# Optimization experiments

Hardware: AMD Instinct MI355X
Metric: run time of the kernel (lower is better)

The kernel has to match this reference:

```python
import jax, jax.numpy as jnp
import numpy as np

N_HEADS = 16
D_HEAD = 64
CHUNK = 64


@jax.custom_vjp
def binarize(x):
    return jnp.where(x >= 0, 1.0, -1.0).astype(x.dtype)

def _bin_fwd(x):
    return binarize(x), x

def _bin_bwd(x, g):
    return (g * (jnp.abs(x) <= 1.0).astype(g.dtype),)

binarize.defvjp(_bin_fwd, _bin_bwd)


def setup_inputs() -> dict:
    key = jax.random.key(0)
    k1, k2, k3 = jax.random.split(key, 3)
    B, T, D = 4, 4096, 1024
    x = jax.random.normal(k1, (B, T, D), dtype=jnp.float32)
    W_qkv = jax.random.normal(k2, (3 * D, D), dtype=jnp.float32) * 0.02
    W_o = jax.random.normal(k3, (D, D), dtype=jnp.float32) * 0.02
    return {"x": x, "W_qkv": W_qkv, "W_o": W_o}


def reference(x, W_qkv, W_o):
    B, T, D = x.shape
    H, d, C = N_HEADS, D_HEAD, CHUNK
    scale = 1.0 / (d ** 0.5)

    qkv = (x @ W_qkv.T).reshape(B, T, 3, H, d)
    q = jnp.swapaxes(qkv[:, :, 0], 1, 2) * scale   # [B,H,T,d]
    k = binarize(jnp.swapaxes(qkv[:, :, 1], 1, 2))
    v = binarize(jnp.swapaxes(qkv[:, :, 2], 1, 2))

    N = T // C  # T chosen divisible by chunk size (pad branch is a no-op)
    qc = q.reshape(B, H, N, C, d)
    kc = k.reshape(B, H, N, C, d)
    vc = v.reshape(B, H, N, C, d)

    mask = jnp.tril(jnp.ones((C, C), dtype=x.dtype))
    intra_scores = jnp.einsum('bhnid,bhnjd->bhnij', qc, kc) * mask
    intra = jnp.einsum('bhnij,bhnjd->bhnid', intra_scores, vc)

    chunk_kv = jnp.einsum('bhnck,bhncd->bhnkd', kc, vc)          # [B,H,N,d,d]
    ckv32 = chunk_kv.astype(jnp.float32)
    prefix = (jnp.cumsum(ckv32, axis=2) - ckv32).astype(chunk_kv.dtype)
    cross = jnp.einsum('bhnck,bhnkd->bhncd', qc, prefix)

    pos = jnp.arange(1, C + 1, dtype=x.dtype)
    offs = jnp.arange(N, dtype=x.dtype) * C
    total = jnp.clip(offs[:, None] + pos[None, :], 1.0, None).reshape(1, 1, N, C, 1)

    out = ((intra + cross) / total).reshape(B, H, T, d)
    out = jnp.swapaxes(out, 1, 2).reshape(B, T, D)
    y = out @ W_o.T

    final_matrix = prefix[:, :, -1] + chunk_kv[:, :, -1]          # [B,H,d,d]
    final_count = jnp.full((B, H, 1, 1), T, dtype=x.dtype)
    return (y, final_matrix, final_count)
```

## Files before the change

### kernel.cpp

```cpp
#include <hip/hip_runtime.h>
#include <cstdint>

#define B_ 4
#define T_ 4096
#define D_ 1024
#define H_ 16
#define HD_ 64
#define N_ 64

typedef __attribute__((ext_vector_type(8))) short s16x8;
typedef __attribute__((ext_vector_type(4))) float f32x4;

__device__ __forceinline__ unsigned short f2bf(float f) {
    unsigned int u = __builtin_bit_cast(unsigned int, f);
    u += 0x7fffu + ((u >> 16) & 1u);
    return (unsigned short)(u >> 16);
}
__device__ __forceinline__ float bf2f(unsigned short h) {
    unsigned int u = ((unsigned int)h) << 16;
    return __builtin_bit_cast(float, u);
}
__device__ __forceinline__ void gl2lds(const short* g, short* l) {
    __builtin_amdgcn_global_load_lds(
        (const __attribute__((address_space(1))) void*)g,
        (__attribute__((address_space(3))) void*)l, 16, 0, 0);
}
#define MFMA16(a, b, c) __builtin_amdgcn_mfma_f32_16x16x32_bf16(a, b, c, 0, 0, 0)
#define SB0() __builtin_amdgcn_sched_barrier(0)
#define BAR() __builtin_amdgcn_s_barrier()

#define BF_P1 ((short)0x3F80)
#define BF_M1 ((short)0xBF80)

__global__ __launch_bounds__(256)
void k_cvt(const float* __restrict__ in, short* __restrict__ out, int n4)
{
    int i = blockIdx.x * blockDim.x + threadIdx.x;
    const int stride = gridDim.x * blockDim.x;
    for (; i < n4; i += stride) {
        float4 f = ((const float4*)in)[i];
        short4 o;
        o.x = (short)f2bf(f.x); o.y = (short)f2bf(f.y);
        o.z = (short)f2bf(f.z); o.w = (short)f2bf(f.w);
        *(short4*)(out + i * 4) = o;
    }
}

template<int MODE, int KD, int NCB>
__global__ __launch_bounds__(512, 4)
void k_gemm2(const short* __restrict__ A, const short* __restrict__ Bm,
             short* __restrict__ Oq, signed char* __restrict__ K8,
             signed char* __restrict__ V8, float* __restrict__ Yf)
{
    __shared__ __align__(16) short LA[256 * 64];
    __shared__ __align__(16) short LB[128 * 64];

    const int tid = threadIdx.x;
    const int nwg = 64 * NCB;
    const int bid = blockIdx.x;
    const int sz  = (bid & 7) * (nwg >> 3) + (bid >> 3);
    const int cb  = sz % NCB, rb = sz / NCB;
    const int row0 = rb * 256, col0 = cb * 128;

    const int lane = tid & 63, w = tid >> 6;
    const int wr = w >> 1, wc = w & 1;
    const int cl = lane & 15, rg = lane >> 4;

    const int sr8 = lane >> 3;
    const int slg = ((lane & 7) ^ sr8) * 8;
    const short* gA = A  + (size_t)(row0 + w * 32 + sr8) * KD + slg;
    const short* gB = Bm + (size_t)(col0 + w * 16 + sr8) * KD + slg;

    f32x4 acc[4][4];
    #pragma unroll
    for (int i = 0; i < 4; ++i)
        #pragma unroll
        for (int j = 0; j < 4; ++j) acc[i][j] = (f32x4)0.f;

    auto stage = [&](int t) {
        const int ko = t * 64;
        #pragma unroll
        for (int c = 0; c < 4; ++c)
            gl2lds(gA + ko + (size_t)c * 8 * KD, &LA[(w * 32 + c * 8) * 64]);
        #pragma unroll
        for (int c = 0; c < 2; ++c)
            gl2lds(gB + ko + (size_t)c * 8 * KD, &LB[(w * 16 + c * 8) * 64]);
    };
    auto ldf = [&](const short* base, int R, int q) -> s16x8 {
        return *(const s16x8*)((const char*)base + R * 128 + ((q ^ (R & 7)) << 4));
    };

    const int nt = KD / 64;
    stage(0);
    for (int t = 0; t < nt; ++t) {
        asm volatile("s_waitcnt vmcnt(0)" ::: "memory");
        BAR();
        SB0();
        #pragma unroll
        for (int kk = 0; kk < 2; ++kk) {
            s16x8 fb[4];
            #pragma unroll
            for (int ni = 0; ni < 4; ++ni)
                fb[ni] = ldf(LB, wc * 64 + ni * 16 + cl, kk * 4 + rg);
            #pragma unroll
            for (int mi = 0; mi < 4; ++mi) {
                s16x8 fa = ldf(LA, wr * 64 + mi * 16 + cl, kk * 4 + rg);
                __builtin_amdgcn_s_setprio(1);
                #pragma unroll
                for (int ni = 0; ni < 4; ++ni)
                    acc[mi][ni] = MFMA16(fa, fb[ni], acc[mi][ni]);
                __builtin_amdgcn_s_setprio(0);
            }
        }
        SB0();
        BAR();
        if (t + 1 < nt) stage(t + 1);
    }

    const int m0 = row0 + wr * 64, n0 = col0 + wc * 64;
    if (MODE == 0) {
        const int s = col0 >> 10;
        #pragma unroll
        for (int ni = 0; ni < 4; ++ni) {
            const int col = n0 + ni * 16 + cl;
            const int h = (col & 1023) >> 6, dd = col & 63;
            #pragma unroll
            for (int mi = 0; mi < 4; ++mi)
                #pragma unroll
                for (int r = 0; r < 4; ++r) {
                    const int bt = m0 + mi * 16 + rg * 4 + r;
                    const int bb = bt >> 12, t = bt & (T_ - 1);
                    const size_t bh64 = (size_t)(bb * H_ + h);
                    const float v = acc[mi][ni][r];
                    if (s == 0) {
                        Oq[(bh64 * T_ + t) * 64 + dd] =
                            (short)f2bf(v * 0.125f);
                    } else if (s == 1) {
                        K8[(bh64 * T_ + t) * 64 + dd] =
                            (v >= 0.f) ? 1 : -1;
                    } else {
                        const size_t otr = bh64 * ((size_t)T_ * 64)
                                         + (size_t)(t >> 6) * 4096 + dd * 64 + (t & 63);
                        V8[otr] = (v >= 0.f) ? 1 : -1;
                    }
                }
        }
    } else {
        #pragma unroll
        for (int ni = 0; ni < 4; ++ni) {
            const int col = n0 + ni * 16 + cl;
            #pragma unroll
            for (int mi = 0; mi < 4; ++mi)
                #pragma unroll
                for (int r = 0; r < 4; ++r)
                    Yf[(size_t)(m0 + mi * 16 + rg * 4 + r) * D_ + col] =
                        acc[mi][ni][r];
        }
    }
}

__global__ __launch_bounds__(256)
void k_chunkA(const signed char* __restrict__ Kb8,
              const signed char* __restrict__ VbT8,
              signed char* __restrict__ CKV8)
{
    __shared__ __align__(16) short KTs[4096], VTs[4096];
    __shared__ __align__(16) signed char Cs8[4096];
    const int tid = threadIdx.x;
    const int bh = blockIdx.x >> 6, n = blockIdx.x & 63;
    const size_t kbase = ((size_t)bh * T_ + n * 64) * 64;
    const size_t vbase = (size_t)bh * T_ * 64 + (size_t)n * 4096;

    {
        const int off = tid * 16;
        int4 vr = *(const int4*)(VbT8 + vbase + off);
        const signed char* vb = (const signed char*)&vr;
        const int vrow = off >> 6, vcb = off & 63;
        #pragma unroll
        for (int jj = 0; jj < 2; ++jj) {
            s16x8 v;
            #pragma unroll
            for (int j = 0; j < 8; ++j)
                v[j] = (vb[jj*8+j] >= 0) ? BF_P1 : BF_M1;
            const int o = (vrow * 128 + (vcb + jj * 8) * 2) ^ ((vrow & 7) << 4);
            *(s16x8*)((char*)VTs + o) = v;
        }
        int4 kr = *(const int4*)(Kb8 + kbase + off);
        const signed char* kb = (const signed char*)&kr;
        const int c = off >> 6, d0 = off & 63;
        #pragma unroll
        for (int j = 0; j < 16; ++j) {
            const int dd = d0 + j;
            const short sv = (kb[j] >= 0) ? BF_P1 : BF_M1;
            const int o2 = (dd * 128 + c * 2) ^ ((dd & 7) << 4);
            *(short*)((char*)KTs + o2) = sv;
        }
    }
    __syncthreads();

    const int lane = tid & 63, w = tid >> 6;
    const int cl = lane & 15, rg = lane >> 4;
    auto frag = [&](const short* l, int rowbase, int kk) -> s16x8 {
        const int row = rowbase + cl;
        int off = row * 128 + kk * 64 + rg * 16;
        off ^= (row & 7) << 4;
        return *(const s16x8*)((const char*)l + off);
    };

    f32x4 a3[4];
    #pragma unroll
    for (int ni = 0; ni < 4; ++ni) a3[ni] = (f32x4)0.f;
    const s16x8 va0 = frag(VTs, w * 16, 0), va1 = frag(VTs, w * 16, 1);
    #pragma unroll
    for (int ni = 0; ni < 4; ++ni) {
        a3[ni] = MFMA16(va0, frag(KTs, ni * 16, 0), a3[ni]);
        a3[ni] = MFMA16(va1, frag(KTs, ni * 16, 1), a3[ni]);
    }
    #pragma unroll
    for (int ni = 0; ni < 4; ++ni)
        #pragma unroll
        for (int r = 0; r < 4; ++r) {
            const int m = w * 16 + rg * 4 + r;
            const int c = ni * 16 + cl;
            Cs8[m * 64 + c] = (signed char)(int)a3[ni][r];
        }
    __syncthreads();
    const size_t c8 = ((size_t)bh * 64 + n) * 4096;
    *(int4*)(CKV8 + c8 + tid * 16) = *(const int4*)(Cs8 + tid * 16);
}

__global__ __launch_bounds__(256)
void k_scan2(const signed char* __restrict__ CKV8, short* __restrict__ PB,
             float* __restrict__ FM, float* __restrict__ FC)
{
    const int bh = blockIdx.x >> 4;
    const int e  = (blockIdx.x & 15) * 256 + threadIdx.x;
    const size_t b8 = (size_t)bh * N_ * 4096 + e;
    const size_t bp = (size_t)bh * N_ * 4096 + e;
    int run = 0;
    #pragma unroll
    for (int nn = 0; nn < 64; ++nn) {
        PB[bp + (size_t)nn * 4096] = (short)f2bf((float)run);
        run += (int)CKV8[b8 + (size_t)nn * 4096];
    }
    FM[(size_t)bh * 4096 + (e & 63) * 64 + (e >> 6)] = (float)run;
    if ((blockIdx.x & 15) == 0 && threadIdx.x == 0) FC[bh] = (float)T_;
}

__global__ __launch_bounds__(256)
void k_cross3(const short* __restrict__ Qb, const signed char* __restrict__ Kb8,
              const signed char* __restrict__ VbT8, const short* __restrict__ PB,
              short* __restrict__ OMb)
{
    __shared__ __align__(16) short Qs[4096], Ks[4096], VTs[4096], Ps[4096], Ss[4096];
    const int tid = threadIdx.x;
    const int bh = blockIdx.x >> 6, n = blockIdx.x & 63;
    const size_t cbase = ((size_t)bh * T_ + n * 64) * 64;
    const size_t kbase = cbase;
    const size_t vbase = (size_t)bh * T_ * 64 + (size_t)n * 4096;

    auto stage_tile = [&](const short* g, short* l) {
        #pragma unroll
        for (int p = 0; p < 2; ++p) {
            const int off = tid * 16 + p * 4096;
            const int r = off >> 7;
            s16x8 v = *(const s16x8*)(g + (off >> 1));
            *(s16x8*)((char*)l + (off ^ ((r & 7) << 4))) = v;
        }
    };
    stage_tile(Qb + cbase, Qs);
    stage_tile(PB + ((size_t)bh * 64 + n) * 4096, Ps);
    {
        const int off = tid * 16;
        int4 kr = *(const int4*)(Kb8 + kbase + off);
        const signed char* kb = (const signed char*)&kr;
        int4 vr = *(const int4*)(VbT8 + vbase + off);
        const signed char* vb = (const signed char*)&vr;
        const int row = off >> 6, cb = off & 63;
        #pragma unroll
        for (int jj = 0; jj < 2; ++jj) {
            s16x8 kv, vv;
            #pragma unroll
            for (int j = 0; j < 8; ++j) {
                kv[j] = (kb[jj*8+j] >= 0) ? BF_P1 : BF_M1;
                vv[j] = (vb[jj*8+j] >= 0) ? BF_P1 : BF_M1;
            }
            const int o = (row * 128 + (cb + jj * 8) * 2) ^ ((row & 7) << 4);
            *(s16x8*)((char*)Ks  + o) = kv;
            *(s16x8*)((char*)VTs + o) = vv;
        }
    }
    __syncthreads();

    const int lane = tid & 63, w = tid >> 6;
    const int cl = lane & 15, rg = lane >> 4;
    auto frag = [&](const short* l, int rowbase, int kk) -> s16x8 {
        const int row = rowbase + cl;
        int off = row * 128 + kk * 64 + rg * 16;
        off ^= (row & 7) << 4;
        return *(const s16x8*)((const char*)l + off);
    };

    const s16x8 qa0 = frag(Qs, w * 16, 0), qa1 = frag(Qs, w * 16, 1);
    {
        f32x4 a1[4];
        #pragma unroll
        for (int ni = 0; ni < 4; ++ni) a1[ni] = (f32x4)0.f;
        #pragma unroll
        for (int ni = 0; ni < 4; ++ni) {
            a1[ni] = MFMA16(qa0, frag(Ks, ni * 16, 0), a1[ni]);
            a1[ni] = MFMA16(qa1, frag(Ks, ni * 16, 1), a1[ni]);
        }
        #pragma unroll
        for (int ni = 0; ni < 4; ++ni)
            #pragma unroll
            for (int r = 0; r < 4; ++r) {
                const int i = w * 16 + rg * 4 + r, j = ni * 16 + cl;
                const float v = (j <= i) ? a1[ni][r] : 0.f;
                const int off = (i * 128 + j * 2) ^ ((i & 7) << 4);
                *(short*)((char*)Ss + off) = (short)f2bf(v);
            }
    }
    __syncthreads();

    {
        f32x4 a2[4], a3[4];
        #pragma unroll
        for (int ni = 0; ni < 4; ++ni) { a2[ni] = (f32x4)0.f; a3[ni] = (f32x4)0.f; }
        const s16x8 sa0 = frag(Ss, w * 16, 0), sa1 = frag(Ss, w * 16, 1);
        #pragma unroll
        for (int ni = 0; ni < 4; ++ni) {
            a2[ni] = MFMA16(sa0, frag(VTs, ni * 16, 0), a2[ni]);
            a2[ni] = MFMA16(sa1, frag(VTs, ni * 16, 1), a2[ni]);
            a3[ni] = MFMA16(qa0, frag(Ps, ni * 16, 0), a3[ni]);
            a3[ni] = MFMA16(qa1, frag(Ps, ni * 16, 1), a3[ni]);
        }
        #pragma unroll
        for (int ni = 0; ni < 4; ++ni)
            #pragma unroll
            for (int r = 0; r < 4; ++r) {
                const int i = w * 16 + rg * 4 + r, j = ni * 16 + cl;
                const float invt = 1.0f / (float)(n * 64 + i + 1);
                const float f = (a2[ni][r] + a3[ni][r]) * invt;
                const int off = (i * 128 + j * 2) ^ ((i & 7) << 4);
                *(short*)((char*)Qs + off) = (short)f2bf(f);
            }
    }
    __syncthreads();

    const int bb = bh >> 4, h = bh & 15;
    #pragma unroll
    for (int p = 0; p < 2; ++p) {
        const int off = tid * 16 + p * 4096;
        const int r = off >> 7;
        const int lo = off ^ ((r & 7) << 4);
        s16x8 v = *(const s16x8*)((char*)Qs + lo);
        const size_t gi = ((size_t)bb * T_ + n * 64 + r) * D_
                        + h * 64 + ((off & 127) >> 1);
        *(s16x8*)(OMb + gi) = v;
    }
}

extern "C" void kernel_launch(void* const* d_in, const int* in_sizes, int n_in,
                              void* d_out, int out_size, void* d_ws, size_t ws_size,
                              hipStream_t stream)
{
    const float* X    = (const float*)d_in[0];
    const float* Wqkv = (const float*)d_in[1];
    const float* Wo   = (const float*)d_in[2];

    float* Y  = (float*)d_out;
    float* FM = Y + (size_t)B_ * T_ * D_;
    float* FC = FM + (size_t)B_ * H_ * HD_ * HD_;

    char* ws = (char*)d_ws;
    const size_t Mi = 1048576;
    short*       Qb     = (short*)(ws + 0 * Mi);
    signed char* Kb8    = (signed char*)(ws + 32 * Mi);
    signed char* VbT8   = (signed char*)(ws + 48 * Mi);
    short*       PB     = (short*)(ws + 64 * Mi);
    short*       Xb     = (short*)(ws + 96 * Mi);
    short*       OMb    = (short*)(ws + 96 * Mi);
    signed char* CKV8   = (signed char*)(ws + 128 * Mi);
    short*       Wqkvb  = (short*)(ws + 144 * Mi);
    short*       WoS    = (short*)(ws + 150 * Mi);
    if (ws_size < (size_t)152 * Mi) return;

    dim3 blk(256), blkg(512);
    k_cvt<<<dim3(2048), blk, 0, stream>>>(X, Xb, 4194304);
    k_cvt<<<dim3(1024), blk, 0, stream>>>(Wqkv, Wqkvb, 786432);
    k_gemm2<0, 1024, 24><<<dim3(1536), blkg, 0, stream>>>(Xb, Wqkvb, Qb, Kb8, VbT8, nullptr);
    k_chunkA<<<dim3(4096), blk, 0, stream>>>(Kb8, VbT8, CKV8);
    k_scan2 <<<dim3(1024), blk, 0, stream>>>(CKV8, PB, FM, FC);
    k_cross3<<<dim3(4096), blk, 0, stream>>>(Qb, Kb8, VbT8, PB, OMb);
    k_cvt<<<dim3(512), blk, 0, stream>>>(Wo, WoS, 262144);
    k_gemm2<1, 1024, 8><<<dim3(512), blkg, 0, stream>>>(OMb, WoS, nullptr, nullptr, nullptr, Y);
}
```

Before: 261.6 us.

## Double-buffer GEMM LDS tiles and shrink to 128x128 tiles with 256 threads

The GEMM kernel moves from a 256x128 tile with 512 threads and a single LDS buffer to a 128x128 tile with 256 threads and two LDS buffers. The next K-slice is loaded into the alternate buffer before waiting, with a partial vmcnt wait, so global-to-LDS loads overlap MFMA work. Grid sizes double to cover the smaller tiles. This trades larger-tile reuse and lower occupancy (launch bounds 256,2) for load/compute overlap.

```diff
diff --git a/kernel.cpp b/kernel.cpp
--- a/kernel.cpp
+++ b/kernel.cpp
@@ -47,20 +47,19 @@
 }
 
 template<int MODE, int KD, int NCB>
-__global__ __launch_bounds__(512, 4)
-void k_gemm2(const short* __restrict__ A, const short* __restrict__ Bm,
+__global__ __launch_bounds__(256, 2)
+void k_gemm3(const short* __restrict__ A, const short* __restrict__ Bm,
              short* __restrict__ Oq, signed char* __restrict__ K8,
              signed char* __restrict__ V8, float* __restrict__ Yf)
 {
-    __shared__ __align__(16) short LA[256 * 64];
-    __shared__ __align__(16) short LB[128 * 64];
+    __shared__ __align__(16) short LS[2][2][8192];
 
     const int tid = threadIdx.x;
-    const int nwg = 64 * NCB;
+    const int nwg = 128 * NCB;
     const int bid = blockIdx.x;
     const int sz  = (bid & 7) * (nwg >> 3) + (bid >> 3);
     const int cb  = sz % NCB, rb = sz / NCB;
-    const int row0 = rb * 256, col0 = cb * 128;
+    const int row0 = rb * 128, col0 = cb * 128;
 
     const int lane = tid & 63, w = tid >> 6;
     const int wr = w >> 1, wc = w & 1;
@@ -69,7 +68,7 @@
     const int sr8 = lane >> 3;
     const int slg = ((lane & 7) ^ sr8) * 8;
     const short* gA = A  + (size_t)(row0 + w * 32 + sr8) * KD + slg;
-    const short* gB = Bm + (size_t)(col0 + w * 16 + sr8) * KD + slg;
+    const short* gB = Bm + (size_t)(col0 + w * 32 + sr8) * KD + slg;
 
     f32x4 acc[4][4];
     #pragma unroll
@@ -77,34 +76,41 @@
         #pragma unroll
         for (int j = 0; j < 4; ++j) acc[i][j] = (f32x4)0.f;
 
-    auto stage = [&](int t) {
+    auto stage = [&](int pb, int t) {
         const int ko = t * 64;
         #pragma unroll
-        for (int c = 0; c < 4; ++c)
-            gl2lds(gA + ko + (size_t)c * 8 * KD, &LA[(w * 32 + c * 8) * 64]);
-        #pragma unroll
-        for (int c = 0; c < 2; ++c)
-            gl2lds(gB + ko + (size_t)c * 8 * KD, &LB[(w * 16 + c * 8) * 64]);
+        for (int c = 0; c < 4; ++c) {
+            gl2lds(gA + ko + (size_t)c * 8 * KD, &LS[pb][0][(w * 32 + c * 8) * 64]);
+            gl2lds(gB + ko + (size_t)c * 8 * KD, &LS[pb][1][(w * 32 + c * 8) * 64]);
+        }
     };
     auto ldf = [&](const short* base, int R, int q) -> s16x8 {
         return *(const s16x8*)((const char*)base + R * 128 + ((q ^ (R & 7)) << 4));
     };
 
     const int nt = KD / 64;
-    stage(0);
+    stage(0, 0);
     for (int t = 0; t < nt; ++t) {
-        asm volatile("s_waitcnt vmcnt(0)" ::: "memory");
+        const int pb = t & 1;
+        if (t + 1 < nt) {
+            stage(pb ^ 1, t + 1);
+            asm volatile("s_waitcnt vmcnt(8)" ::: "memory");
+        } else {
+            asm volatile("s_waitcnt vmcnt(0)" ::: "memory");
+        }
         BAR();
         SB0();
+        const short* bA = &LS[pb][0][0];
+        const short* bB = &LS[pb][1][0];
         #pragma unroll
         for (int kk = 0; kk < 2; ++kk) {
             s16x8 fb[4];
             #pragma unroll
             for (int ni = 0; ni < 4; ++ni)
-                fb[ni] = ldf(LB, wc * 64 + ni * 16 + cl, kk * 4 + rg);
+                fb[ni] = ldf(bB, wc * 64 + ni * 16 + cl, kk * 4 + rg);
             #pragma unroll
             for (int mi = 0; mi < 4; ++mi) {
-                s16x8 fa = ldf(LA, wr * 64 + mi * 16 + cl, kk * 4 + rg);
+                s16x8 fa = ldf(bA, wr * 64 + mi * 16 + cl, kk * 4 + rg);
                 __builtin_amdgcn_s_setprio(1);
                 #pragma unroll
                 for (int ni = 0; ni < 4; ++ni)
@@ -114,7 +120,6 @@
         }
         SB0();
         BAR();
-        if (t + 1 < nt) stage(t + 1);
     }
 
     const int m0 = row0 + wr * 64, n0 = col0 + wc * 64;
@@ -386,13 +391,13 @@
     short*       WoS    = (short*)(ws + 150 * Mi);
     if (ws_size < (size_t)152 * Mi) return;
 
-    dim3 blk(256), blkg(512);
+    dim3 blk(256);
     k_cvt<<<dim3(2048), blk, 0, stream>>>(X, Xb, 4194304);
     k_cvt<<<dim3(1024), blk, 0, stream>>>(Wqkv, Wqkvb, 786432);
-    k_gemm2<0, 1024, 24><<<dim3(1536), blkg, 0, stream>>>(Xb, Wqkvb, Qb, Kb8, VbT8, nullptr);
+    k_gemm3<0, 1024, 24><<<dim3(3072), blk, 0, stream>>>(Xb, Wqkvb, Qb, Kb8, VbT8, nullptr);
     k_chunkA<<<dim3(4096), blk, 0, stream>>>(Kb8, VbT8, CKV8);
     k_scan2 <<<dim3(1024), blk, 0, stream>>>(CKV8, PB, FM, FC);
     k_cross3<<<dim3(4096), blk, 0, stream>>>(Qb, Kb8, VbT8, PB, OMb);
     k_cvt<<<dim3(512), blk, 0, stream>>>(Wo, WoS, 262144);
-    k_gemm2<1, 1024, 8><<<dim3(512), blkg, 0, stream>>>(OMb, WoS, nullptr, nullptr, nullptr, Y);
-}
+    k_gemm3<1, 1024, 8><<<dim3(1024), blk, 0, stream>>>(OMb, WoS, nullptr, nullptr, nullptr, Y);
+}
```

Result: slower. 269.9 us (+3.2%).
